# Performance work log

Measured on AMD Instinct MI355X. Metric: run time of the kernel, lower is better.

The kernel has to match this reference:

```python
import jax, jax.numpy as jnp
import numpy as np

NUM_NODES = 40000
NUM_EDGES = 400000
DIM = 128
NUM_REL = 502  # num_relation * 2
NUM_HEAD = 1


def setup_inputs() -> dict:
    key = jax.random.key(0)
    ks = jax.random.split(key, 16)
    d = DIM
    return {
        "curr_stat": jax.random.normal(ks[0], (NUM_NODES, d), jnp.float32),
        "last_stat": jax.random.normal(ks[1], (NUM_NODES, d), jnp.float32),
        "relemb_weight": jax.random.normal(ks[2], (NUM_REL, d), jnp.float32),
        "selfrel_weight": jax.random.normal(ks[3], (1, d), jnp.float32),
        "Wq": jax.random.normal(ks[4], (2 * d, d), jnp.float32) * (1.0 / np.sqrt(2 * d)),
        "bq": jax.random.normal(ks[5], (d,), jnp.float32) * 0.02,
        "Wk": jax.random.normal(ks[6], (2 * d, d), jnp.float32) * (1.0 / np.sqrt(2 * d)),
        "bk": jax.random.normal(ks[7], (d,), jnp.float32) * 0.02,
        "Wv": jax.random.normal(ks[8], (d, d), jnp.float32) * (1.0 / np.sqrt(d)),
        "bv": jax.random.normal(ks[9], (d,), jnp.float32) * 0.02,
        "dyn_weight": jax.random.normal(ks[10], (d, d), jnp.float32) * (1.0 / np.sqrt(d)),
        "edge_index": jax.random.randint(ks[11], (2, NUM_EDGES), 0, NUM_NODES, jnp.int32),
        "edge_type": jax.random.randint(ks[12], (NUM_EDGES,), 0, NUM_REL, jnp.int32),
    }


def _segment_softmax(scores, seg, num_segments):
    # scores: [E, H]; softmax over edges sharing the same destination segment
    m = jax.ops.segment_max(scores, seg, num_segments=num_segments)  # [N, H]
    e = jnp.exp(scores - m[seg])
    s = jax.ops.segment_sum(e, seg, num_segments=num_segments)  # [N, H]
    return e / s[seg]


def reference(curr_stat, last_stat, relemb_weight, selfrel_weight,
              Wq, bq, Wk, bk, Wv, bv, dyn_weight,
              edge_index, edge_type):
    N, D = curr_stat.shape
    H = NUM_HEAD
    HD = D // H

    # append self-loop edges for every node, with the dedicated self-relation
    loop = jnp.arange(N, dtype=edge_index.dtype)
    src = jnp.concatenate([edge_index[0], loop])  # [E_total]
    dst = jnp.concatenate([edge_index[1], loop])  # [E_total]
    type_emb = jnp.concatenate(
        [relemb_weight[edge_type], jnp.broadcast_to(selfrel_weight, (N, D))], axis=0)

    E = src.shape[0]
    # linear projections (x @ W + b); torch Linear stores W transposed, same math
    q = (jnp.concatenate([curr_stat[dst], type_emb], -1) @ Wq + bq).reshape(E, H, HD)
    k = (jnp.concatenate([last_stat[src], type_emb], -1) @ Wk + bk).reshape(E, H, HD)
    v = (last_stat[src] @ Wv + bv).reshape(E, H, HD)

    attn = jnp.sum(q * k, axis=-1) / np.sqrt(HD).astype(np.float32)  # [E, H]

    dyn_prob = _segment_softmax(attn, dst, N)   # [E, H]
    sta_prob = _segment_softmax(-attn, dst, N)  # [E, H]

    counts = jax.ops.segment_sum(jnp.ones((E,), jnp.float32), dst, num_segments=N)
    denom = jnp.maximum(counts, 1.0)[:, None]  # scatter-mean denominator

    feat_dyn = jax.ops.segment_sum((dyn_prob[..., None] * v).reshape(E, D), dst,
                                   num_segments=N) / denom
    feat_sta = jax.ops.segment_sum((sta_prob[..., None] * v).reshape(E, D), dst,
                                   num_segments=N) / denom

    # stack (feat_sta, feat_dyn @ dyn_weight) -> [2, N, D]
    return jnp.stack([feat_sta, feat_dyn @ dyn_weight])
```

## Files before the change

kernel.cpp:

```cpp
#include <hip/hip_runtime.h>
#include <hip/hip_bf16.h>
#include <math.h>

#define DIMC 128
#define CS2L (0.08838834764831845f * 1.4426950408889634f)

typedef __attribute__((ext_vector_type(8))) short short8;
typedef __attribute__((ext_vector_type(4))) float floatx4;
typedef __attribute__((ext_vector_type(2))) float f32x2;

static __device__ __forceinline__ unsigned pk2(float lo, float hi) {
    __hip_bfloat162 h = __float22bfloat162_rn(make_float2(lo, hi));
    return *(unsigned*)&h;
}
static __device__ __forceinline__ unsigned short f2bf(float x) {
    union { float f; unsigned int u; } v; v.f = x;
    unsigned int r = v.u + 0x7FFFu + ((v.u >> 16) & 1u);
    return (unsigned short)(r >> 16);
}
static __device__ __forceinline__ f32x2 bfp(unsigned int u) {
    union { unsigned int i; float f; } a, b;
    a.i = u << 16; b.i = u & 0xFFFF0000u;
    f32x2 r; r.x = a.f; r.y = b.f; return r;
}

template<int CTRL>
static __device__ __forceinline__ float dpp_add(float x) {
    int y = __builtin_amdgcn_update_dpp(0, __float_as_int(x), CTRL, 0xF, 0xF, true);
    return x + __int_as_float(y);
}
static __device__ __forceinline__ float red16(float p) {
    p = dpp_add<0xB1>(p);
    p = dpp_add<0x4E>(p);
    p = dpp_add<0x141>(p);
    p = dpp_add<0x140>(p);
    return p;
}

struct PrepArgs {
    const float* W[6];
    unsigned short* F[6];
    float wscale[6];
    const float* relemb; const float* selfrel;
    float* TypeEmb;
    int* deg;
    int R; int N;
};

__global__ __launch_bounds__(64) void prep_all(PrepArgs a)
{
    int b = blockIdx.x;
    int lane = threadIdx.x;
    if (b < 192) {
        int mat = b >> 5, ts = b & 31;
        int s = ts & 3, t = ts >> 2;
        int q = lane >> 4, c = lane & 15;
        const float* W = a.W[mat];
        float sc = a.wscale[mat];
        unsigned short o[8];
        #pragma unroll
        for (int j = 0; j < 8; ++j)
            o[j] = f2bf(W[(long)(s * 32 + q * 8 + j) * DIMC + t * 16 + c] * sc);
        uint4 u;
        u.x = (unsigned)o[0] | ((unsigned)o[1] << 16);
        u.y = (unsigned)o[2] | ((unsigned)o[3] << 16);
        u.z = (unsigned)o[4] | ((unsigned)o[5] << 16);
        u.w = (unsigned)o[6] | ((unsigned)o[7] << 16);
        ((uint4*)a.F[mat])[ts * 64 + lane] = u;
    } else if (b < 192 + a.R + 1) {
        int r = b - 192;
        const float* src = (r < a.R) ? (a.relemb + (long)r * DIMC) : a.selfrel;
        float2 v = ((const float2*)src)[lane];
        ((float2*)(a.TypeEmb + (long)r * DIMC))[lane] = v;
    } else {
        int i = (b - (192 + a.R + 1)) * 64 + lane;
        if (i < a.N) a.deg[i] = 0;
    }
}

struct GemmM5 {
    const float*          Af[5];
    const unsigned short* Ab[5];
    const unsigned short* F[5];
    const float*          bias[5];
    float                 bscale[5];
    float*                outf[5];
    unsigned short*       outb[5];
    int                   ostride[5];
    int                   ooff[5];
    int                   M[5];
    const int*            hist_dst;
    int*                  hist_deg;
    int                   hist_E;
};

__global__ __launch_bounds__(256) void gemm_mfma(GemmM5 g)
{
    if (blockIdx.y == 5) {
        int i = blockIdx.x * blockDim.x + threadIdx.x;
        int stride = gridDim.x * blockDim.x;
        for (; i < g.hist_E; i += stride) atomicAdd(&g.hist_deg[g.hist_dst[i]], 1);
        return;
    }

    const int which = blockIdx.y;
    const int M = g.M[which];
    if (blockIdx.x * 64 >= M) return;

    const float*          __restrict__ Af   = g.Af[which];
    const unsigned short* __restrict__ Ab   = g.Ab[which];
    const unsigned short* __restrict__ F    = g.F[which];
    const float*          __restrict__ bias = g.bias[which];
    const float bsc = g.bscale[which];
    float*          __restrict__ outf = g.outf[which];
    unsigned short* __restrict__ outb = g.outb[which];
    const int ostride = g.ostride[which];
    const int ooff    = g.ooff[which];

    const int wave = threadIdx.x >> 6;
    const int lane = threadIdx.x & 63;
    const int q = lane >> 4, c = lane & 15;
    const int rowbase = blockIdx.x * 64 + wave * 16;

    short8 wf[8][4];
    const uint4* Fp = (const uint4*)F;
    #pragma unroll
    for (int t = 0; t < 8; ++t)
        #pragma unroll
        for (int s = 0; s < 4; ++s) {
            uint4 u = Fp[(t * 4 + s) * 64 + lane];
            wf[t][s] = *(short8*)&u;
        }

    floatx4 acc[8];
    #pragma unroll
    for (int t = 0; t < 8; ++t) {
        float b = bias ? bias[t * 16 + c] * bsc : 0.0f;
        acc[t] = (floatx4){b, b, b, b};
    }

    int rowA = rowbase + c; if (rowA > M - 1) rowA = M - 1;
    short8 af[4];
    if (Af) {
        const float* Ar = Af + (long)rowA * DIMC + q * 8;
        #pragma unroll
        for (int s = 0; s < 4; ++s) {
            float4 x0 = *(const float4*)(Ar + s * 32);
            float4 x1 = *(const float4*)(Ar + s * 32 + 4);
            uint4 u;
            u.x = pk2(x0.x, x0.y);
            u.y = pk2(x0.z, x0.w);
            u.z = pk2(x1.x, x1.y);
            u.w = pk2(x1.z, x1.w);
            af[s] = *(short8*)&u;
        }
    } else {
        const unsigned short* Ar = Ab + (long)rowA * DIMC + q * 8;
        #pragma unroll
        for (int s = 0; s < 4; ++s) {
            uint4 u = *(const uint4*)(Ar + s * 32);
            af[s] = *(short8*)&u;
        }
    }

    #pragma unroll
    for (int t = 0; t < 8; ++t)
        #pragma unroll
        for (int s = 0; s < 4; ++s)
            acc[t] = __builtin_amdgcn_mfma_f32_16x16x32_bf16(af[s], wf[t][s], acc[t], 0, 0, 0);

    if (outf) {
        #pragma unroll
        for (int t = 0; t < 8; ++t)
            #pragma unroll
            for (int r = 0; r < 4; ++r) {
                int row = rowbase + q * 4 + r;
                if (row < M)
                    outf[(long)row * DIMC + t * 16 + c] = acc[t][r];
            }
    } else {
        #pragma unroll
        for (int t = 0; t < 8; ++t)
            #pragma unroll
            for (int r = 0; r < 4; ++r) {
                float other = __shfl_xor(acc[t][r], 1);
                int row = rowbase + q * 4 + r;
                if ((lane & 1) == 0 && row < M) {
                    unsigned word = pk2(acc[t][r], other);
                    ((unsigned*)outb)[((long)row * 64 + t * 8 + (c >> 1))
                                      * (long)ostride + ooff] = word;
                }
            }
    }
}

__global__ __launch_bounds__(256) void partial_sums(const int* __restrict__ deg,
                                                    int* __restrict__ partial, int N)
{
    __shared__ int sh[256];
    int t = threadIdx.x;
    int beg = blockIdx.x * 1024 + t * 4;
    int s = 0;
    if (beg + 3 < N) { int4 v = *(const int4*)(deg + beg); s = v.x + v.y + v.z + v.w; }
    else { for (int j = 0; j < 4; ++j) if (beg + j < N) s += deg[beg + j]; }
    sh[t] = s;
    __syncthreads();
    for (int d = 128; d >= 1; d >>= 1) {
        if (t < d) sh[t] += sh[t + d];
        __syncthreads();
    }
    if (t == 0) partial[blockIdx.x] = sh[0];
}

__global__ __launch_bounds__(256) void scan_write_offsets(const int* __restrict__ deg,
                                                          const int* __restrict__ partial,
                                                          int* __restrict__ offs,
                                                          int* __restrict__ cursor, int N, int nb)
{
    __shared__ int sh[256];
    __shared__ int sbase;
    int t = threadIdx.x;
    if (t < 64) {
        int v = (t < nb && t < (int)blockIdx.x) ? partial[t] : 0;
        #pragma unroll
        for (int d = 32; d >= 1; d >>= 1) v += __shfl_xor(v, d);
        if (t == 0) sbase = v;
    }
    int beg = blockIdx.x * 1024 + t * 4;
    int d0 = 0, d1 = 0, d2 = 0, d3 = 0;
    if (beg + 3 < N) { int4 v = *(const int4*)(deg + beg); d0 = v.x; d1 = v.y; d2 = v.z; d3 = v.w; }
    else {
        if (beg < N)     d0 = deg[beg];
        if (beg + 1 < N) d1 = deg[beg + 1];
        if (beg + 2 < N) d2 = deg[beg + 2];
        if (beg + 3 < N) d3 = deg[beg + 3];
    }
    int s = d0 + d1 + d2 + d3;
    sh[t] = s;
    __syncthreads();
    for (int d = 1; d < 256; d <<= 1) {
        int v = (t >= d) ? sh[t - d] : 0;
        __syncthreads();
        sh[t] += v;
        __syncthreads();
    }
    int base = sbase + sh[t] - s;
    int o0 = base, o1 = o0 + d0, o2 = o1 + d1, o3 = o2 + d2;
    if (beg < N)     { offs[beg]     = o0; cursor[beg]     = o0; }
    if (beg + 1 < N) { offs[beg + 1] = o1; cursor[beg + 1] = o1; }
    if (beg + 2 < N) { offs[beg + 2] = o2; cursor[beg + 2] = o2; }
    if (beg + 3 < N) { offs[beg + 3] = o3; cursor[beg + 3] = o3; }
}

__global__ void scatter_kernel(const int* __restrict__ src, const int* __restrict__ dst,
                               const int* __restrict__ etype, int* __restrict__ cursor,
                               int2* __restrict__ sedge, int E)
{
    int e = blockIdx.x * blockDim.x + threadIdx.x;
    if (e < E) {
        int d = dst[e];
        int p = atomicAdd(&cursor[d], 1);
        sedge[p] = make_int2(src[e] << 8, etype[e] << 9);
    }
}

__global__ __launch_bounds__(256) void node_kernel(
    const float* __restrict__ Qn,
    const char*  __restrict__ Kb,
    const char*  __restrict__ Vb,
    const char*  __restrict__ QKb,
    const int* __restrict__ offs, const int* __restrict__ deg,
    const int2* __restrict__ sedge,
    float* __restrict__ out_sta, uint4* __restrict__ feat_dyn,
    int N, int R)
{
    int n = (blockIdx.x * blockDim.x + threadIdx.x) >> 6;
    int lane = threadIdx.x & 63;
    if (n >= N) return;
    const int ql = lane & 15;
    const int qt = lane >> 4;
    const int lo16 = ql << 4;
    const int lo32 = ql << 5;

    int base = offs[n];
    int dcnt = deg[n];
    int etot = dcnt + 1;

    const float4* qp = (const float4*)(Qn + (long)n * DIMC + ql * 8);
    float4 qa = qp[0], qb = qp[1];
    f32x2 q01; q01.x = qa.x; q01.y = qa.y;
    f32x2 q23; q23.x = qa.z; q23.y = qa.w;
    f32x2 q45; q45.x = qb.x; q45.y = qb.y;
    f32x2 q67; q67.x = qb.z; q67.y = qb.w;

    float s_d = 0.0f, s_s = 0.0f;
    f32x2 accd0 = {0.f, 0.f}, accd1 = accd0, accd2 = accd0, accd3 = accd0;
    f32x2 accs0 = accd0, accs1 = accd0, accs2 = accd0, accs3 = accd0;

    const int selfK = n << 8, selfQ = R << 9;

    int T = (etot + 3) >> 2;
    for (int it = 0; it < T; ++it) {
        int i = 4 * it + qt;
        bool vv = i < etot;
        bool re = i < dcnt;
        int2 e = re ? sedge[base + i] : make_int2(selfK, selfQ);

        uint4 kx  = *(const uint4*)(Kb + e.x + lo16);
        uint4 vx  = *(const uint4*)(Vb + e.x + lo16);
        uint4 qk0 = *(const uint4*)(QKb + e.y + lo32);
        uint4 qk1 = *(const uint4*)(QKb + e.y + lo32 + 16);

        f32x2 a0 = q01 + bfp(qk0.x), a1 = q23 + bfp(qk0.z);
        f32x2 a2 = q45 + bfp(qk1.x), a3 = q67 + bfp(qk1.z);
        f32x2 k0 = bfp(kx.x) + bfp(qk0.y), k1 = bfp(kx.y) + bfp(qk0.w);
        f32x2 k2 = bfp(kx.z) + bfp(qk1.y), k3 = bfp(kx.w) + bfp(qk1.w);
        f32x2 dp = a0 * k0;
        dp += a1 * k1;
        dp += a2 * k2;
        dp += a3 * k3;
        float p = red16(dp.x + dp.y);

        float wd = vv ? exp2f(p)  : 0.0f;
        float ws = vv ? exp2f(-p) : 0.0f;
        s_d += wd; s_s += ws;

        f32x2 v0 = bfp(vx.x), v1 = bfp(vx.y), v2 = bfp(vx.z), v3 = bfp(vx.w);
        accd0 += v0 * wd; accd1 += v1 * wd; accd2 += v2 * wd; accd3 += v3 * wd;
        accs0 += v0 * ws; accs1 += v1 * ws; accs2 += v2 * ws; accs3 += v3 * ws;
    }

    #define MRG(x) { x += __shfl_xor(x, 16); x += __shfl_xor(x, 32); }
    MRG(s_d) MRG(s_s)
    MRG(accd0.x) MRG(accd0.y) MRG(accd1.x) MRG(accd1.y)
    MRG(accd2.x) MRG(accd2.y) MRG(accd3.x) MRG(accd3.y)
    MRG(accs0.x) MRG(accs0.y) MRG(accs1.x) MRG(accs1.y)
    MRG(accs2.x) MRG(accs2.y) MRG(accs3.x) MRG(accs3.y)
    #undef MRG

    if (qt == 0) {
        float denom = (float)(dcnt + 1);
        float id_ = 1.0f / (s_d * denom);
        float is_ = 1.0f / (s_s * denom);
        float4* op = (float4*)(out_sta + (long)n * DIMC + ql * 8);
        op[0] = make_float4(accs0.x * is_, accs0.y * is_, accs1.x * is_, accs1.y * is_);
        op[1] = make_float4(accs2.x * is_, accs2.y * is_, accs3.x * is_, accs3.y * is_);
        uint4 w;
        w.x = pk2(accd0.x * id_, accd0.y * id_);
        w.y = pk2(accd1.x * id_, accd1.y * id_);
        w.z = pk2(accd2.x * id_, accd2.y * id_);
        w.w = pk2(accd3.x * id_, accd3.y * id_);
        feat_dyn[(unsigned)n * 16u + ql] = w;
    }
}

extern "C" void kernel_launch(void* const* d_in, const int* in_sizes, int n_in,
                              void* d_out, int out_size, void* d_ws, size_t ws_size,
                              hipStream_t stream)
{
    const float* curr    = (const float*)d_in[0];
    const float* last    = (const float*)d_in[1];
    const float* relemb  = (const float*)d_in[2];
    const float* selfrel = (const float*)d_in[3];
    const float* Wq      = (const float*)d_in[4];
    const float* bq      = (const float*)d_in[5];
    const float* Wk      = (const float*)d_in[6];
    const float* bk      = (const float*)d_in[7];
    const float* Wv      = (const float*)d_in[8];
    const float* bv      = (const float*)d_in[9];
    const float* dynw    = (const float*)d_in[10];
    const int*   eidx    = (const int*)d_in[11];
    const int*   etype   = (const int*)d_in[12];
    float* out = (float*)d_out;

    const int N = in_sizes[0] / DIMC;
    const int E = in_sizes[12];
    const int R = in_sizes[2] / DIMC;
    const int* esrc = eidx;
    const int* edst = eidx + E;

    char* wp = (char*)d_ws;
    auto alloc = [&](size_t bytes) { char* r = wp; wp += (bytes + 15) & ~(size_t)15; return r; };
    size_t nd = (size_t)N * DIMC;
    float*          Qn    = (float*)alloc(nd * 4);
    unsigned short* Kb    = (unsigned short*)alloc((size_t)N * 256);
    unsigned short* Vb    = (unsigned short*)alloc((size_t)N * 256);
    unsigned short* Fdb   = (unsigned short*)alloc(nd * 2);
    uint4*          QKre  = (uint4*)alloc((size_t)(R + 1) * 32 * 16);
    float*          TypeEmb = (float*)alloc((size_t)(R + 2) * DIMC * 4);
    unsigned short* FW[6];
    for (int m = 0; m < 6; ++m) FW[m] = (unsigned short*)alloc(2048 * 8 * 2);
    int*            deg   = (int*)alloc((size_t)N * 4);
    int*            offs  = (int*)alloc((size_t)N * 4);
    int*            cursor= (int*)alloc((size_t)N * 4);
    int2*           sedge = (int2*)alloc((size_t)E * 8);
    int*            partial = (int*)alloc(256 * 4);

    const int gblk = N / 64;
    const int sblk = (N + 1023) / 1024;

    PrepArgs pa;
    pa.W[0] = Wq;   pa.W[1] = Wk;   pa.W[2] = Wv;
    pa.W[3] = dynw; pa.W[4] = Wq + (size_t)DIMC * DIMC; pa.W[5] = Wk + (size_t)DIMC * DIMC;
    pa.wscale[0] = CS2L; pa.wscale[1] = 1.0f; pa.wscale[2] = 1.0f;
    pa.wscale[3] = 1.0f; pa.wscale[4] = CS2L; pa.wscale[5] = 1.0f;
    for (int m = 0; m < 6; ++m) pa.F[m] = FW[m];
    pa.relemb = relemb; pa.selfrel = selfrel; pa.TypeEmb = TypeEmb;
    pa.deg = deg; pa.R = R; pa.N = N;
    int pgrid = 192 + (R + 1) + (N + 63) / 64;
    hipLaunchKernelGGL(prep_all, dim3(pgrid), dim3(64), 0, stream, pa);

    GemmM5 g5;
    for (int s = 0; s < 5; ++s) { g5.Ab[s] = nullptr; g5.outf[s] = nullptr; g5.outb[s] = nullptr; g5.bscale[s] = 1.0f; }
    g5.Af[0] = curr;    g5.F[0] = FW[0]; g5.bias[0] = nullptr; g5.outf[0] = Qn;
    g5.ostride[0] = 1;  g5.ooff[0] = 0;  g5.M[0] = N;
    g5.Af[1] = last;    g5.F[1] = FW[1]; g5.bias[1] = nullptr; g5.outb[1] = Kb;
    g5.ostride[1] = 1;  g5.ooff[1] = 0;  g5.M[1] = N;
    g5.Af[2] = last;    g5.F[2] = FW[2]; g5.bias[2] = bv;      g5.outb[2] = Vb;
    g5.ostride[2] = 1;  g5.ooff[2] = 0;  g5.M[2] = N;
    g5.Af[3] = TypeEmb; g5.F[3] = FW[4]; g5.bias[3] = bq;      g5.outb[3] = (unsigned short*)QKre;
    g5.ostride[3] = 2;  g5.ooff[3] = 0;  g5.M[3] = R + 1;      g5.bscale[3] = CS2L;
    g5.Af[4] = TypeEmb; g5.F[4] = FW[5]; g5.bias[4] = bk;      g5.outb[4] = (unsigned short*)QKre;
    g5.ostride[4] = 2;  g5.ooff[4] = 1;  g5.M[4] = R + 1;
    g5.hist_dst = edst; g5.hist_deg = deg; g5.hist_E = E;
    hipLaunchKernelGGL(gemm_mfma, dim3(gblk, 6), dim3(256), 0, stream, g5);

    hipLaunchKernelGGL(partial_sums, dim3(sblk), dim3(256), 0, stream, deg, partial, N);
    hipLaunchKernelGGL(scan_write_offsets, dim3(sblk), dim3(256), 0, stream,
                       deg, partial, offs, cursor, N, sblk);
    hipLaunchKernelGGL(scatter_kernel, dim3((E + 255) / 256), dim3(256), 0, stream,
                       esrc, edst, etype, cursor, sedge, E);

    hipLaunchKernelGGL(node_kernel, dim3((N + 3) / 4), dim3(256), 0, stream,
                       Qn, (const char*)Kb, (const char*)Vb, (const char*)QKre,
                       offs, deg, sedge, out, (uint4*)Fdb, N, R);

    GemmM5 gf;
    for (int s = 0; s < 5; ++s) { gf.Af[s] = nullptr; gf.Ab[s] = nullptr; gf.outf[s] = nullptr; gf.outb[s] = nullptr; gf.M[s] = 0; gf.bscale[s] = 1.0f; }
    gf.Ab[0] = Fdb; gf.F[0] = FW[3]; gf.bias[0] = nullptr; gf.outf[0] = out + nd;
    gf.ostride[0] = 1; gf.ooff[0] = 0; gf.M[0] = N;
    gf.hist_dst = edst; gf.hist_deg = deg; gf.hist_E = 0;
    hipLaunchKernelGGL(gemm_mfma, dim3(gblk, 1), dim3(256), 0, stream, gf);
}
```

Before: 224.7 us.

## Replace global-atomic histogram and scatter with range-partitioned LDS atomics; stage weights in LDS

Degree counting and the CSR edge scatter now use 128 blocks, each owning a contiguous range of destination nodes. Each block scans all edges and does its atomics on a shared-memory counter array, instead of global atomics on every edge. This removes the deg zeroing and the separate cursor array. In exchange, every block rereads the full edge list (about 128x redundant reads of dst), and the edge order within a segment changes. The GEMM also stages its bf16 weight fragments in LDS instead of holding them in registers, which cuts VGPR pressure but adds a barrier and 32 KB of LDS per block.

```diff
diff --git a/kernel.cpp b/kernel.cpp
--- a/kernel.cpp
+++ b/kernel.cpp
@@ -4,6 +4,8 @@
 
 #define DIMC 128
 #define CS2L (0.08838834764831845f * 1.4426950408889634f)
+#define HB   128
+#define HRNG 320
 
 typedef __attribute__((ext_vector_type(8))) short short8;
 typedef __attribute__((ext_vector_type(4))) float floatx4;
@@ -43,8 +45,7 @@
     float wscale[6];
     const float* relemb; const float* selfrel;
     float* TypeEmb;
-    int* deg;
-    int R; int N;
+    int R;
 };
 
 __global__ __launch_bounds__(64) void prep_all(PrepArgs a)
@@ -67,14 +68,11 @@
         u.z = (unsigned)o[4] | ((unsigned)o[5] << 16);
         u.w = (unsigned)o[6] | ((unsigned)o[7] << 16);
         ((uint4*)a.F[mat])[ts * 64 + lane] = u;
-    } else if (b < 192 + a.R + 1) {
+    } else {
         int r = b - 192;
         const float* src = (r < a.R) ? (a.relemb + (long)r * DIMC) : a.selfrel;
         float2 v = ((const float2*)src)[lane];
         ((float2*)(a.TypeEmb + (long)r * DIMC))[lane] = v;
-    } else {
-        int i = (b - (192 + a.R + 1)) * 64 + lane;
-        if (i < a.N) a.deg[i] = 0;
     }
 }
 
@@ -92,20 +90,47 @@
     const int*            hist_dst;
     int*                  hist_deg;
     int                   hist_E;
+    int                   hist_N;
+    int                   hist_rpb;
 };
 
 __global__ __launch_bounds__(256) void gemm_mfma(GemmM5 g)
 {
+    __shared__ uint4 wlds[2048];
+    __shared__ int   lh[HRNG];
+
     if (blockIdx.y == 5) {
-        int i = blockIdx.x * blockDim.x + threadIdx.x;
-        int stride = gridDim.x * blockDim.x;
-        for (; i < g.hist_E; i += stride) atomicAdd(&g.hist_deg[g.hist_dst[i]], 1);
+        int b = blockIdx.x;
+        if (b >= HB) return;
+        int tid = threadIdx.x;
+        int lo = b * g.hist_rpb;
+        for (int i = tid; i < HRNG; i += 256) lh[i] = 0;
+        __syncthreads();
+        const int4* p4 = (const int4*)g.hist_dst;
+        int nv = g.hist_E >> 2;
+        unsigned rng = (unsigned)g.hist_rpb;
+        for (int i = tid; i < nv; i += 256) {
+            int4 v = p4[i];
+            unsigned r;
+            r = (unsigned)(v.x - lo); if (r < rng) atomicAdd(&lh[r], 1);
+            r = (unsigned)(v.y - lo); if (r < rng) atomicAdd(&lh[r], 1);
+            r = (unsigned)(v.z - lo); if (r < rng) atomicAdd(&lh[r], 1);
+            r = (unsigned)(v.w - lo); if (r < rng) atomicAdd(&lh[r], 1);
+        }
+        for (int i = (nv << 2) + tid; i < g.hist_E; i += 256) {
+            unsigned r = (unsigned)(g.hist_dst[i] - lo);
+            if (r < rng) atomicAdd(&lh[r], 1);
+        }
+        __syncthreads();
+        int cap = g.hist_N - lo;
+        for (int i = tid; i < g.hist_rpb; i += 256)
+            if (i < cap) g.hist_deg[lo + i] = lh[i];
         return;
     }
 
     const int which = blockIdx.y;
     const int M = g.M[which];
-    if (blockIdx.x * 64 >= M) return;
+    if ((int)blockIdx.x * 64 >= M) return;
 
     const float*          __restrict__ Af   = g.Af[which];
     const unsigned short* __restrict__ Ab   = g.Ab[which];
@@ -122,21 +147,11 @@
     const int q = lane >> 4, c = lane & 15;
     const int rowbase = blockIdx.x * 64 + wave * 16;
 
-    short8 wf[8][4];
-    const uint4* Fp = (const uint4*)F;
-    #pragma unroll
-    for (int t = 0; t < 8; ++t)
-        #pragma unroll
-        for (int s = 0; s < 4; ++s) {
-            uint4 u = Fp[(t * 4 + s) * 64 + lane];
-            wf[t][s] = *(short8*)&u;
-        }
-
-    floatx4 acc[8];
-    #pragma unroll
-    for (int t = 0; t < 8; ++t) {
-        float b = bias ? bias[t * 16 + c] * bsc : 0.0f;
-        acc[t] = (floatx4){b, b, b, b};
+    {
+        const uint4* Fp = (const uint4*)F;
+        #pragma unroll
+        for (int j = 0; j < 8; ++j)
+            wlds[threadIdx.x + j * 256] = Fp[threadIdx.x + j * 256];
     }
 
     int rowA = rowbase + c; if (rowA > M - 1) rowA = M - 1;
@@ -163,11 +178,22 @@
         }
     }
 
+    floatx4 acc[8];
+    #pragma unroll
+    for (int t = 0; t < 8; ++t) {
+        float b = bias ? bias[t * 16 + c] * bsc : 0.0f;
+        acc[t] = (floatx4){b, b, b, b};
+    }
+
+    __syncthreads();
+
     #pragma unroll
     for (int t = 0; t < 8; ++t)
         #pragma unroll
-        for (int s = 0; s < 4; ++s)
-            acc[t] = __builtin_amdgcn_mfma_f32_16x16x32_bf16(af[s], wf[t][s], acc[t], 0, 0, 0);
+        for (int s = 0; s < 4; ++s) {
+            uint4 u = wlds[(t * 4 + s) * 64 + lane];
+            acc[t] = __builtin_amdgcn_mfma_f32_16x16x32_bf16(af[s], *(short8*)&u, acc[t], 0, 0, 0);
+        }
 
     if (outf) {
         #pragma unroll
@@ -215,7 +241,7 @@
 __global__ __launch_bounds__(256) void scan_write_offsets(const int* __restrict__ deg,
                                                           const int* __restrict__ partial,
                                                           int* __restrict__ offs,
-                                                          int* __restrict__ cursor, int N, int nb)
+                                                          int N, int nb)
 {
     __shared__ int sh[256];
     __shared__ int sbase;
@@ -246,21 +272,38 @@
     }
     int base = sbase + sh[t] - s;
     int o0 = base, o1 = o0 + d0, o2 = o1 + d1, o3 = o2 + d2;
-    if (beg < N)     { offs[beg]     = o0; cursor[beg]     = o0; }
-    if (beg + 1 < N) { offs[beg + 1] = o1; cursor[beg + 1] = o1; }
-    if (beg + 2 < N) { offs[beg + 2] = o2; cursor[beg + 2] = o2; }
-    if (beg + 3 < N) { offs[beg + 3] = o3; cursor[beg + 3] = o3; }
-}
-
-__global__ void scatter_kernel(const int* __restrict__ src, const int* __restrict__ dst,
-                               const int* __restrict__ etype, int* __restrict__ cursor,
-                               int2* __restrict__ sedge, int E)
-{
-    int e = blockIdx.x * blockDim.x + threadIdx.x;
-    if (e < E) {
-        int d = dst[e];
-        int p = atomicAdd(&cursor[d], 1);
-        sedge[p] = make_int2(src[e] << 8, etype[e] << 9);
+    if (beg < N)     offs[beg]     = o0;
+    if (beg + 1 < N) offs[beg + 1] = o1;
+    if (beg + 2 < N) offs[beg + 2] = o2;
+    if (beg + 3 < N) offs[beg + 3] = o3;
+}
+
+__global__ __launch_bounds__(256) void scatter_range(
+    const int* __restrict__ esrc, const int* __restrict__ edst,
+    const int* __restrict__ etype, const int* __restrict__ offs,
+    int2* __restrict__ sedge, int E, int N, int rpb)
+{
+    __shared__ int lcur[HRNG];
+    int b = blockIdx.x, tid = threadIdx.x;
+    int lo = b * rpb;
+    for (int i = tid; i < HRNG; i += 256)
+        lcur[i] = (i < rpb && lo + i < N) ? offs[lo + i] : 0;
+    __syncthreads();
+    const int4* p4 = (const int4*)edst;
+    int nv = E >> 2;
+    unsigned rng = (unsigned)rpb;
+    for (int i = tid; i < nv; i += 256) {
+        int4 v = p4[i];
+        int e0 = 4 * i;
+        unsigned r;
+        r = (unsigned)(v.x - lo); if (r < rng) { int p = atomicAdd(&lcur[r], 1); sedge[p] = make_int2(esrc[e0] << 8, etype[e0] << 9); }
+        r = (unsigned)(v.y - lo); if (r < rng) { int p = atomicAdd(&lcur[r], 1); sedge[p] = make_int2(esrc[e0 + 1] << 8, etype[e0 + 1] << 9); }
+        r = (unsigned)(v.z - lo); if (r < rng) { int p = atomicAdd(&lcur[r], 1); sedge[p] = make_int2(esrc[e0 + 2] << 8, etype[e0 + 2] << 9); }
+        r = (unsigned)(v.w - lo); if (r < rng) { int p = atomicAdd(&lcur[r], 1); sedge[p] = make_int2(esrc[e0 + 3] << 8, etype[e0 + 3] << 9); }
+    }
+    for (int i = (nv << 2) + tid; i < E; i += 256) {
+        unsigned r = (unsigned)(edst[i] - lo);
+        if (r < rng) { int p = atomicAdd(&lcur[r], 1); sedge[p] = make_int2(esrc[i] << 8, etype[i] << 9); }
     }
 }
 
@@ -392,12 +435,12 @@
     for (int m = 0; m < 6; ++m) FW[m] = (unsigned short*)alloc(2048 * 8 * 2);
     int*            deg   = (int*)alloc((size_t)N * 4);
     int*            offs  = (int*)alloc((size_t)N * 4);
-    int*            cursor= (int*)alloc((size_t)N * 4);
     int2*           sedge = (int2*)alloc((size_t)E * 8);
     int*            partial = (int*)alloc(256 * 4);
 
     const int gblk = N / 64;
     const int sblk = (N + 1023) / 1024;
+    const int rpb  = (N + HB - 1) / HB;
 
     PrepArgs pa;
     pa.W[0] = Wq;   pa.W[1] = Wk;   pa.W[2] = Wv;
@@ -406,9 +449,8 @@
     pa.wscale[3] = 1.0f; pa.wscale[4] = CS2L; pa.wscale[5] = 1.0f;
     for (int m = 0; m < 6; ++m) pa.F[m] = FW[m];
     pa.relemb = relemb; pa.selfrel = selfrel; pa.TypeEmb = TypeEmb;
-    pa.deg = deg; pa.R = R; pa.N = N;
-    int pgrid = 192 + (R + 1) + (N + 63) / 64;
-    hipLaunchKernelGGL(prep_all, dim3(pgrid), dim3(64), 0, stream, pa);
+    pa.R = R;
+    hipLaunchKernelGGL(prep_all, dim3(192 + R + 1), dim3(64), 0, stream, pa);
 
     GemmM5 g5;
     for (int s = 0; s < 5; ++s) { g5.Ab[s] = nullptr; g5.outf[s] = nullptr; g5.outb[s] = nullptr; g5.bscale[s] = 1.0f; }
@@ -422,14 +464,14 @@
     g5.ostride[3] = 2;  g5.ooff[3] = 0;  g5.M[3] = R + 1;      g5.bscale[3] = CS2L;
     g5.Af[4] = TypeEmb; g5.F[4] = FW[5]; g5.bias[4] = bk;      g5.outb[4] = (unsigned short*)QKre;
     g5.ostride[4] = 2;  g5.ooff[4] = 1;  g5.M[4] = R + 1;
-    g5.hist_dst = edst; g5.hist_deg = deg; g5.hist_E = E;
+    g5.hist_dst = edst; g5.hist_deg = deg; g5.hist_E = E; g5.hist_N = N; g5.hist_rpb = rpb;
     hipLaunchKernelGGL(gemm_mfma, dim3(gblk, 6), dim3(256), 0, stream, g5);
 
     hipLaunchKernelGGL(partial_sums, dim3(sblk), dim3(256), 0, stream, deg, partial, N);
     hipLaunchKernelGGL(scan_write_offsets, dim3(sblk), dim3(256), 0, stream,
-                       deg, partial, offs, cursor, N, sblk);
-    hipLaunchKernelGGL(scatter_kernel, dim3((E + 255) / 256), dim3(256), 0, stream,
-                       esrc, edst, etype, cursor, sedge, E);
+                       deg, partial, offs, N, sblk);
+    hipLaunchKernelGGL(scatter_range, dim3(HB), dim3(256), 0, stream,
+                       esrc, edst, etype, offs, sedge, E, N, rpb);
 
     hipLaunchKernelGGL(node_kernel, dim3((N + 3) / 4), dim3(256), 0, stream,
                        Qn, (const char*)Kb, (const char*)Vb, (const char*)QKre,
@@ -439,6 +481,6 @@
     for (int s = 0; s < 5; ++s) { gf.Af[s] = nullptr; gf.Ab[s] = nullptr; gf.outf[s] = nullptr; gf.outb[s] = nullptr; gf.M[s] = 0; gf.bscale[s] = 1.0f; }
     gf.Ab[0] = Fdb; gf.F[0] = FW[3]; gf.bias[0] = nullptr; gf.outf[0] = out + nd;
     gf.ostride[0] = 1; gf.ooff[0] = 0; gf.M[0] = N;
-    gf.hist_dst = edst; gf.hist_deg = deg; gf.hist_E = 0;
+    gf.hist_dst = edst; gf.hist_deg = deg; gf.hist_E = 0; gf.hist_N = N; gf.hist_rpb = rpb;
     hipLaunchKernelGGL(gemm_mfma, dim3(gblk, 1), dim3(256), 0, stream, gf);
 }
```

Result: slower. 526.0 us (+134.0%).
